# Kernel tuning notes

Hardware: AMD Instinct MI355X
Metric: run time of the kernel (lower is better)

The kernel has to match this reference:

```python
import jax, jax.numpy as jnp
import numpy as np

N, K, D = 65536, 1024, 512


def setup_inputs() -> dict:
    key = jax.random.key(0)
    k1, k2, k3 = jax.random.split(key, 3)
    x = jax.random.normal(k1, (N, D), dtype=jnp.float32)
    y = jax.random.randint(k2, (N,), 0, K)  # true/assigned cluster labels
    centers = jax.random.normal(k3, (K, D), dtype=jnp.float32)  # nn.Parameter
    return {"x": x, "y": y, "centers": centers}


def reference(x, y, centers):
    # caldis: squared euclidean distance from every point to every center.
    # original expand+sub+square+sum without materializing [N, K, D]).
    x2 = jnp.sum(x * x, axis=1, keepdims=True)          # [N, 1]
    c2 = jnp.sum(centers * centers, axis=1)              # [K]
    distance = x2 - 2.0 * (x @ centers.T) + c2           # [N, K]

    # predict: torch.sort(distance)[1][:, 0] == index of the smallest distance
    ynew = jnp.argmin(distance, axis=1)                  # [N]

    # calwei + calloss: one-hot(y) * distance summed == gather distance[i, y[i]]
    loss = jnp.sum(jnp.take_along_axis(distance, y[:, None], axis=1))

    return loss, ynew
```

## Files before the change

### kernel.cpp

```cpp
#include <hip/hip_runtime.h>

#define NPTS 65536
#define KC   1024
#define DD   512

using bf16x8 = __attribute__((ext_vector_type(8))) __bf16;
using f32x4  = __attribute__((ext_vector_type(4))) float;

__device__ __forceinline__ void gld_lds16(const void* g, void* lds_base) {
  __builtin_amdgcn_global_load_lds(
      (const __attribute__((address_space(1))) unsigned int*)(uintptr_t)g,
      (__attribute__((address_space(3))) unsigned int*)(unsigned int)(uintptr_t)lds_base,
      16, 0, 0);
}

__device__ __forceinline__ uint2 pack4(const float4& v) {
  uint2 r;
  r.x = (__float_as_uint(v.x) >> 16) | (__float_as_uint(v.y) & 0xffff0000u);
  r.y = (__float_as_uint(v.z) >> 16) | (__float_as_uint(v.w) & 0xffff0000u);
  return r;
}


__global__ __launch_bounds__(256) void convert_x_loss(
    const float* __restrict__ x, const int* __restrict__ y,
    const float* __restrict__ centers, uint4* __restrict__ xb,
    float* __restrict__ partial) {
  const int w = threadIdx.x >> 6, l = threadIdx.x & 63;
  const int base = blockIdx.x * 64 + w * 16;
  const float4* xf4 = (const float4*)x;
  const float4* cf4 = (const float4*)centers;
  float s = 0.f;
  for (int p = 0; p < 16; p++) {
    const int row = base + p;
    float4 a = xf4[row * 128 + 2 * l];
    float4 b = xf4[row * 128 + 2 * l + 1];
    uint2 pa = pack4(a), pb = pack4(b);
    xb[row * 64 + l] = make_uint4(pa.x, pa.y, pb.x, pb.y);
    const int yr = y[row];
    float4 ca = cf4[yr * 128 + 2 * l];
    float4 cb = cf4[yr * 128 + 2 * l + 1];
    float d0 = a.x - ca.x, d1 = a.y - ca.y, d2 = a.z - ca.z, d3 = a.w - ca.w;
    float d4 = b.x - cb.x, d5 = b.y - cb.y, d6 = b.z - cb.z, d7 = b.w - cb.w;
    s += d0 * d0 + d1 * d1 + d2 * d2 + d3 * d3;
    s += d4 * d4 + d5 * d5 + d6 * d6 + d7 * d7;
  }
#pragma unroll
  for (int off = 32; off; off >>= 1) s += __shfl_down(s, off, 64);
  __shared__ float ps[4];
  if (l == 0) ps[w] = s;
  __syncthreads();
  if (threadIdx.x == 0) partial[blockIdx.x] = ps[0] + ps[1] + ps[2] + ps[3];
}

__global__ __launch_bounds__(256) void convert_c(
    const float* __restrict__ centers, uint4* __restrict__ cb,
    float* __restrict__ c2) {
  const int row = (blockIdx.x * 256 + threadIdx.x) >> 6;
  const int l = threadIdx.x & 63;
  const float4* cf4 = (const float4*)centers;
  float4 a = cf4[row * 128 + 2 * l];
  float4 b = cf4[row * 128 + 2 * l + 1];
  uint2 pa = pack4(a), pb = pack4(b);
  cb[row * 64 + l] = make_uint4(pa.x, pa.y, pb.x, pb.y);
  float s = a.x * a.x + a.y * a.y + a.z * a.z + a.w * a.w +
            b.x * b.x + b.y * b.y + b.z * b.z + b.w * b.w;
#pragma unroll
  for (int off = 32; off; off >>= 1) s += __shfl_down(s, off, 64);
  if (l == 0) c2[row] = s;
}

__global__ __launch_bounds__(256, 2) void gemm_argmin(
    const uint4* __restrict__ xb, const uint4* __restrict__ cb,
    const float* __restrict__ c2, float* __restrict__ ynew_out) {
  __shared__ uint4 As[1024];
  __shared__ uint4 Bs[1024];
  __shared__ float c2s[1024];

  const int t = threadIdx.x;
  const int w = t >> 6, l = t & 63;
  const int wm = w >> 1, wn = w & 1;
  const int q4 = l >> 4, m16 = l & 15;
  const int row0 = blockIdx.x * 128;

#pragma unroll
  for (int i = 0; i < 4; i++) c2s[t + 256 * i] = c2[t + 256 * i];

  const int r_l = l >> 3;
  const int o_l = (l & 7) ^ r_l;
  int aidx[4], bidx[4];
#pragma unroll
  for (int q = 0; q < 4; q++) {
    const int c = w * 4 + q;
    aidx[q] = (row0 + c * 8 + r_l) * 64 + o_l;
    bidx[q] = (c * 8 + r_l) * 64 + o_l;
  }

  const int xr = m16 & 7;

  float best[16];
  int bi_[16];
#pragma unroll
  for (int i = 0; i < 16; i++) { best[i] = 3.4e38f; bi_[i] = 0; }

  for (int n0 = 0; n0 < KC; n0 += 128) {
    f32x4 acc[4][4];
#pragma unroll
    for (int i = 0; i < 4; i++)
#pragma unroll
      for (int j = 0; j < 4; j++) acc[i][j] = (f32x4){0.f, 0.f, 0.f, 0.f};

    const uint4* bbase = cb + n0 * 64;

    for (int ks = 0; ks < 8; ks++) {
      __syncthreads();
#pragma unroll
      for (int q = 0; q < 4; q++) {
        gld_lds16(xb + aidx[q] + ks * 8, &As[(w * 4 + q) * 64]);
        gld_lds16(bbase + bidx[q] + ks * 8, &Bs[(w * 4 + q) * 64]);
      }
      __syncthreads();
#pragma unroll
      for (int kk = 0; kk < 2; kk++) {
        bf16x8 af[4], bf[4];
        const int oct = kk * 4 + q4;
#pragma unroll
        for (int i = 0; i < 4; i++) {
          const int ra = wm * 64 + i * 16 + m16;
          af[i] = *(const bf16x8*)&As[ra * 8 + (oct ^ xr)];
          const int rb = wn * 64 + i * 16 + m16;
          bf[i] = *(const bf16x8*)&Bs[rb * 8 + (oct ^ xr)];
        }
#pragma unroll
        for (int i = 0; i < 4; i++)
#pragma unroll
          for (int j = 0; j < 4; j++)
            acc[i][j] = __builtin_amdgcn_mfma_f32_16x16x32_bf16(af[i], bf[j], acc[i][j], 0, 0, 0);
      }
    }

#pragma unroll
    for (int j = 0; j < 4; j++) {
      const int n = n0 + wn * 64 + j * 16 + m16;
      const float cc = c2s[n];
#pragma unroll
      for (int i = 0; i < 4; i++)
#pragma unroll
        for (int r = 0; r < 4; r++) {
          float v = fmaf(-2.f, acc[i][j][r], cc);
          const int bi = i * 4 + r;
          if (v < best[bi]) { best[bi] = v; bi_[bi] = n; }
        }
    }
  }

#pragma unroll
  for (int bi = 0; bi < 16; bi++) {
    float v = best[bi];
    int idx = bi_[bi];
#pragma unroll
    for (int off = 8; off; off >>= 1) {
      float ov = __shfl_xor(v, off, 64);
      int oi = __shfl_xor(idx, off, 64);
      if (ov < v || (ov == v && oi < idx)) { v = ov; idx = oi; }
    }
    if (m16 == 0) {
      const int m = wm * 64 + (bi >> 2) * 16 + q4 * 4 + (bi & 3);
      ynew_out[row0 + m] = (float)idx;
    }
  }
}

__global__ __launch_bounds__(256) void loss_final(const float* __restrict__ partial,
                                                  float* __restrict__ out) {
  float s = 0.f;
#pragma unroll
  for (int j = 0; j < 4; j++) s += partial[threadIdx.x + 256 * j];
#pragma unroll
  for (int off = 32; off; off >>= 1) s += __shfl_down(s, off, 64);
  __shared__ float ps[4];
  if ((threadIdx.x & 63) == 0) ps[threadIdx.x >> 6] = s;
  __syncthreads();
  if (threadIdx.x == 0) out[0] = ps[0] + ps[1] + ps[2] + ps[3];
}


#define SLOT(row, oct) (16 * (oct) + (((row) & 15) ^ (((oct) & 2) << 1)))

__device__ __forceinline__ void split_pack(const float4& a, const float4& b,
                                           uint4& hi, uint4& lo) {
  float f[8] = {a.x, a.y, a.z, a.w, b.x, b.y, b.z, b.w};
  uint hw[4], lw[4];
#pragma unroll
  for (int i = 0; i < 4; i++) {
    uint e0 = __float_as_uint(f[2 * i]), e1 = __float_as_uint(f[2 * i + 1]);
    hw[i] = (e0 >> 16) | (e1 & 0xffff0000u);
    float l0 = f[2 * i]     - __uint_as_float(e0 & 0xffff0000u);
    float l1 = f[2 * i + 1] - __uint_as_float(e1 & 0xffff0000u);
    lw[i] = (__float_as_uint(l0) >> 16) | (__float_as_uint(l1) & 0xffff0000u);
  }
  hi = make_uint4(hw[0], hw[1], hw[2], hw[3]);
  lo = make_uint4(lw[0], lw[1], lw[2], lw[3]);
}

__global__ __launch_bounds__(256) void c2_kernel(const float* __restrict__ centers,
                                                 float* __restrict__ c2) {
  int wave = (blockIdx.x * 256 + threadIdx.x) >> 6;
  int lane = threadIdx.x & 63;
  const float4* c4 = (const float4*)(centers + (size_t)wave * DD);
  float s = 0.f;
#pragma unroll
  for (int j = 0; j < 2; j++) {
    float4 v = c4[lane + 64 * j];
    s += v.x * v.x + v.y * v.y + v.z * v.z + v.w * v.w;
  }
#pragma unroll
  for (int off = 32; off; off >>= 1) s += __shfl_down(s, off, 64);
  if (lane == 0) c2[wave] = s;
}

__global__ __launch_bounds__(256, 2) void argmin_fb(
    const float* __restrict__ x, const float* __restrict__ centers,
    const float* __restrict__ c2, float* __restrict__ ynew_out) {
  __shared__ uint4 Ah[512], Al[512], Bh[512], Bl[512];
  const int t = threadIdx.x;
  const int w = t >> 6, l = t & 63;
  const int wm = w >> 1, wn = w & 1;
  const size_t row0 = (size_t)blockIdx.x * 128;
  const int srow = t >> 1, h = t & 1;
  const int mt = srow >> 4;
  const int so0 = mt * 64 + SLOT(srow, 2 * h);
  const int so1 = mt * 64 + SLOT(srow, 2 * h + 1);
  const int rs = SLOT(l & 15, l >> 4);
  const float* xp = x + (row0 + srow) * DD + h * 16;
  float best[16];
  int bidx[16];
#pragma unroll
  for (int i = 0; i < 16; i++) { best[i] = 3.4e38f; bidx[i] = 0; }
  for (int n0 = 0; n0 < KC; n0 += 128) {
    const float* bp = centers + (size_t)(n0 + srow) * DD + h * 16;
    f32x4 acc[4][4];
#pragma unroll
    for (int i = 0; i < 4; i++)
#pragma unroll
      for (int j = 0; j < 4; j++) acc[i][j] = (f32x4){0.f, 0.f, 0.f, 0.f};
    float4 ra[4], rb[4];
#pragma unroll
    for (int q = 0; q < 4; q++) {
      ra[q] = *(const float4*)(xp + q * 4);
      rb[q] = *(const float4*)(bp + q * 4);
    }
    for (int ks = 0; ks < 16; ks++) {
      uint4 ah0, al0, ah1, al1, bh0, bl0, bh1, bl1;
      split_pack(ra[0], ra[1], ah0, al0);
      split_pack(ra[2], ra[3], ah1, al1);
      split_pack(rb[0], rb[1], bh0, bl0);
      split_pack(rb[2], rb[3], bh1, bl1);
      __syncthreads();
      Ah[so0] = ah0; Al[so0] = al0;
      Ah[so1] = ah1; Al[so1] = al1;
      Bh[so0] = bh0; Bl[so0] = bl0;
      Bh[so1] = bh1; Bl[so1] = bl1;
      __syncthreads();
      if (ks < 15) {
#pragma unroll
        for (int q = 0; q < 4; q++) {
          ra[q] = *(const float4*)(xp + (ks + 1) * 32 + q * 4);
          rb[q] = *(const float4*)(bp + (ks + 1) * 32 + q * 4);
        }
      }
      bf16x8 afh[4], afl[4], bfh[4], bfl[4];
#pragma unroll
      for (int i = 0; i < 4; i++) {
        afh[i] = *(const bf16x8*)&Ah[(wm * 4 + i) * 64 + rs];
        afl[i] = *(const bf16x8*)&Al[(wm * 4 + i) * 64 + rs];
        bfh[i] = *(const bf16x8*)&Bh[(wn * 4 + i) * 64 + rs];
        bfl[i] = *(const bf16x8*)&Bl[(wn * 4 + i) * 64 + rs];
      }
#pragma unroll
      for (int i = 0; i < 4; i++)
#pragma unroll
        for (int j = 0; j < 4; j++) {
          acc[i][j] = __builtin_amdgcn_mfma_f32_16x16x32_bf16(afh[i], bfh[j], acc[i][j], 0, 0, 0);
          acc[i][j] = __builtin_amdgcn_mfma_f32_16x16x32_bf16(afl[i], bfh[j], acc[i][j], 0, 0, 0);
          acc[i][j] = __builtin_amdgcn_mfma_f32_16x16x32_bf16(afh[i], bfl[j], acc[i][j], 0, 0, 0);
        }
    }
#pragma unroll
    for (int j = 0; j < 4; j++) {
      int n = n0 + wn * 64 + j * 16 + (l & 15);
      float cc = c2[n];
#pragma unroll
      for (int i = 0; i < 4; i++)
#pragma unroll
        for (int r = 0; r < 4; r++) {
          float v = fmaf(-2.f, acc[i][j][r], cc);
          int bi = i * 4 + r;
          if (v < best[bi]) { best[bi] = v; bidx[bi] = n; }
        }
    }
  }
#pragma unroll
  for (int bi = 0; bi < 16; bi++) {
    float v = best[bi];
    int idx = bidx[bi];
#pragma unroll
    for (int off = 8; off; off >>= 1) {
      float ov = __shfl_xor(v, off, 64);
      int oi = __shfl_xor(idx, off, 64);
      if (ov < v || (ov == v && oi < idx)) { v = ov; idx = oi; }
    }
    if ((l & 15) == 0) {
      int m = wm * 64 + (bi >> 2) * 16 + (l >> 4) * 4 + (bi & 3);
      ynew_out[row0 + m] = (float)idx;
    }
  }
}

__global__ __launch_bounds__(256) void loss_partial_fb(
    const float* __restrict__ x, const int* __restrict__ y,
    const float* __restrict__ centers, float* __restrict__ partial) {
  const int w = threadIdx.x >> 6, l = threadIdx.x & 63;
  const int base = blockIdx.x * 64 + w * 16;
  float s = 0.f;
  for (int p = 0; p < 16; p++) {
    int i = base + p;
    const float4* x4 = (const float4*)(x + (size_t)i * DD);
    const float4* c4 = (const float4*)(centers + (size_t)y[i] * DD);
#pragma unroll
    for (int j = 0; j < 2; j++) {
      float4 xv = x4[l + 64 * j], cv = c4[l + 64 * j];
      float dx = xv.x - cv.x, dy = xv.y - cv.y, dz = xv.z - cv.z, dw = xv.w - cv.w;
      s += dx * dx + dy * dy + dz * dz + dw * dw;
    }
  }
#pragma unroll
  for (int off = 32; off; off >>= 1) s += __shfl_down(s, off, 64);
  __shared__ float ps[4];
  if (l == 0) ps[w] = s;
  __syncthreads();
  if (threadIdx.x == 0) partial[blockIdx.x] = ps[0] + ps[1] + ps[2] + ps[3];
}


extern "C" void kernel_launch(void* const* d_in, const int* in_sizes, int n_in,
                              void* d_out, int out_size, void* d_ws, size_t ws_size,
                              hipStream_t stream) {
  const float* x       = (const float*)d_in[0];
  const int*   y       = (const int*)d_in[1];
  const float* centers = (const float*)d_in[2];
  float* out = (float*)d_out;

  const size_t xb_bytes = (size_t)NPTS * DD * 2;
  const size_t cb_bytes = (size_t)KC * DD * 2;
  const size_t need = xb_bytes + cb_bytes + (KC + 1024) * sizeof(float);

  if (ws_size >= need) {
    uint4* xb      = (uint4*)d_ws;
    uint4* cbp     = (uint4*)((char*)d_ws + xb_bytes);
    float* c2      = (float*)((char*)d_ws + xb_bytes + cb_bytes);
    float* partial = c2 + KC;
    convert_c<<<KC / 4, 256, 0, stream>>>(centers, cbp, c2);
    convert_x_loss<<<NPTS / 64, 256, 0, stream>>>(x, y, centers, xb, partial);
    gemm_argmin<<<NPTS / 128, 256, 0, stream>>>(xb, cbp, c2, out + 1);
    loss_final<<<1, 256, 0, stream>>>(partial, out);
  } else {
    float* c2      = (float*)d_ws;
    float* partial = c2 + KC;
    c2_kernel<<<KC / 4, 256, 0, stream>>>(centers, c2);
    argmin_fb<<<NPTS / 128, 256, 0, stream>>>(x, centers, c2, out + 1);
    loss_partial_fb<<<NPTS / 64, 256, 0, stream>>>(x, y, centers, partial);
    loss_final<<<1, 256, 0, stream>>>(partial, out);
  }
}
```

Before: 289.2 us.

## Widen GEMM N-tile to 256 and spread conversion kernel across more blocks

The argmin GEMM now processes 256 centers per outer iteration instead of 128. Each wave computes a 64x128 sub-tile with 32 accumulators, so A fragments are reused across twice as many MFMAs and the A tile is reloaded half as often. The x conversion and loss kernels now give one row per wave instead of 16, launching 16384 blocks for more parallelism, and the partial-sum buffer and final reduction grow to match. The larger accumulator set and doubled B LDS buffer raise register and shared-memory pressure, which may reduce occupancy under the launch bound of 2.

```diff
diff --git a/kernel.cpp b/kernel.cpp
--- a/kernel.cpp
+++ b/kernel.cpp
@@ -27,24 +27,20 @@
     const float* __restrict__ centers, uint4* __restrict__ xb,
     float* __restrict__ partial) {
   const int w = threadIdx.x >> 6, l = threadIdx.x & 63;
-  const int base = blockIdx.x * 64 + w * 16;
-  const float4* xf4 = (const float4*)x;
-  const float4* cf4 = (const float4*)centers;
-  float s = 0.f;
-  for (int p = 0; p < 16; p++) {
-    const int row = base + p;
-    float4 a = xf4[row * 128 + 2 * l];
-    float4 b = xf4[row * 128 + 2 * l + 1];
-    uint2 pa = pack4(a), pb = pack4(b);
-    xb[row * 64 + l] = make_uint4(pa.x, pa.y, pb.x, pb.y);
-    const int yr = y[row];
-    float4 ca = cf4[yr * 128 + 2 * l];
-    float4 cb = cf4[yr * 128 + 2 * l + 1];
-    float d0 = a.x - ca.x, d1 = a.y - ca.y, d2 = a.z - ca.z, d3 = a.w - ca.w;
-    float d4 = b.x - cb.x, d5 = b.y - cb.y, d6 = b.z - cb.z, d7 = b.w - cb.w;
-    s += d0 * d0 + d1 * d1 + d2 * d2 + d3 * d3;
-    s += d4 * d4 + d5 * d5 + d6 * d6 + d7 * d7;
-  }
+  const int row = blockIdx.x * 4 + w;
+  const float4* xr = (const float4*)(x + (size_t)row * DD);
+  float4 a = xr[2 * l];
+  float4 b = xr[2 * l + 1];
+  uint2 pa = pack4(a), pb = pack4(b);
+  xb[row * 64 + l] = make_uint4(pa.x, pa.y, pb.x, pb.y);
+  const int yr = y[row];
+  const float4* cr = (const float4*)(centers + (size_t)yr * DD);
+  float4 ca = cr[2 * l];
+  float4 cb = cr[2 * l + 1];
+  float d0 = a.x - ca.x, d1 = a.y - ca.y, d2 = a.z - ca.z, d3 = a.w - ca.w;
+  float d4 = b.x - cb.x, d5 = b.y - cb.y, d6 = b.z - cb.z, d7 = b.w - cb.w;
+  float s = d0 * d0 + d1 * d1 + d2 * d2 + d3 * d3 +
+            d4 * d4 + d5 * d5 + d6 * d6 + d7 * d7;
 #pragma unroll
   for (int off = 32; off; off >>= 1) s += __shfl_down(s, off, 64);
   __shared__ float ps[4];
@@ -74,7 +70,7 @@
     const uint4* __restrict__ xb, const uint4* __restrict__ cb,
     const float* __restrict__ c2, float* __restrict__ ynew_out) {
   __shared__ uint4 As[1024];
-  __shared__ uint4 Bs[1024];
+  __shared__ uint4 Bs[2048];
   __shared__ float c2s[1024];
 
   const int t = threadIdx.x;
@@ -88,13 +84,14 @@
 
   const int r_l = l >> 3;
   const int o_l = (l & 7) ^ r_l;
-  int aidx[4], bidx[4];
-#pragma unroll
-  for (int q = 0; q < 4; q++) {
-    const int c = w * 4 + q;
-    aidx[q] = (row0 + c * 8 + r_l) * 64 + o_l;
-    bidx[q] = (c * 8 + r_l) * 64 + o_l;
-  }
+  int aidx[4];
+#pragma unroll
+  for (int q = 0; q < 4; q++)
+    aidx[q] = (row0 + (w * 4 + q) * 8 + r_l) * 64 + o_l;
+  int bsrc[8];
+#pragma unroll
+  for (int q = 0; q < 8; q++)
+    bsrc[q] = ((w * 8 + q) * 8 + r_l) * 64 + o_l;
 
   const int xr = m16 & 7;
 
@@ -103,45 +100,47 @@
 #pragma unroll
   for (int i = 0; i < 16; i++) { best[i] = 3.4e38f; bi_[i] = 0; }
 
-  for (int n0 = 0; n0 < KC; n0 += 128) {
-    f32x4 acc[4][4];
+  for (int n0 = 0; n0 < KC; n0 += 256) {
+    f32x4 acc[4][8];
 #pragma unroll
     for (int i = 0; i < 4; i++)
 #pragma unroll
-      for (int j = 0; j < 4; j++) acc[i][j] = (f32x4){0.f, 0.f, 0.f, 0.f};
+      for (int j = 0; j < 8; j++) acc[i][j] = (f32x4){0.f, 0.f, 0.f, 0.f};
 
     const uint4* bbase = cb + n0 * 64;
 
     for (int ks = 0; ks < 8; ks++) {
       __syncthreads();
 #pragma unroll
-      for (int q = 0; q < 4; q++) {
+      for (int q = 0; q < 4; q++)
         gld_lds16(xb + aidx[q] + ks * 8, &As[(w * 4 + q) * 64]);
-        gld_lds16(bbase + bidx[q] + ks * 8, &Bs[(w * 4 + q) * 64]);
-      }
+#pragma unroll
+      for (int q = 0; q < 8; q++)
+        gld_lds16(bbase + bsrc[q] + ks * 8, &Bs[(w * 8 + q) * 64]);
       __syncthreads();
 #pragma unroll
       for (int kk = 0; kk < 2; kk++) {
-        bf16x8 af[4], bf[4];
         const int oct = kk * 4 + q4;
+        bf16x8 af[4];
 #pragma unroll
         for (int i = 0; i < 4; i++) {
           const int ra = wm * 64 + i * 16 + m16;
           af[i] = *(const bf16x8*)&As[ra * 8 + (oct ^ xr)];
-          const int rb = wn * 64 + i * 16 + m16;
-          bf[i] = *(const bf16x8*)&Bs[rb * 8 + (oct ^ xr)];
-        }
-#pragma unroll
-        for (int i = 0; i < 4; i++)
-#pragma unroll
-          for (int j = 0; j < 4; j++)
-            acc[i][j] = __builtin_amdgcn_mfma_f32_16x16x32_bf16(af[i], bf[j], acc[i][j], 0, 0, 0);
+        }
+#pragma unroll
+        for (int j = 0; j < 8; j++) {
+          const int rb = wn * 128 + j * 16 + m16;
+          bf16x8 bf = *(const bf16x8*)&Bs[rb * 8 + (oct ^ xr)];
+#pragma unroll
+          for (int i = 0; i < 4; i++)
+            acc[i][j] = __builtin_amdgcn_mfma_f32_16x16x32_bf16(af[i], bf, acc[i][j], 0, 0, 0);
+        }
       }
     }
 
 #pragma unroll
-    for (int j = 0; j < 4; j++) {
-      const int n = n0 + wn * 64 + j * 16 + m16;
+    for (int j = 0; j < 8; j++) {
+      const int n = n0 + wn * 128 + j * 16 + m16;
       const float cc = c2s[n];
 #pragma unroll
       for (int i = 0; i < 4; i++)
@@ -175,7 +174,7 @@
                                                   float* __restrict__ out) {
   float s = 0.f;
 #pragma unroll
-  for (int j = 0; j < 4; j++) s += partial[threadIdx.x + 256 * j];
+  for (int j = 0; j < 64; j++) s += partial[threadIdx.x + 256 * j];
 #pragma unroll
   for (int off = 32; off; off >>= 1) s += __shfl_down(s, off, 64);
   __shared__ float ps[4];
@@ -321,18 +320,15 @@
     const float* __restrict__ x, const int* __restrict__ y,
     const float* __restrict__ centers, float* __restrict__ partial) {
   const int w = threadIdx.x >> 6, l = threadIdx.x & 63;
-  const int base = blockIdx.x * 64 + w * 16;
+  const int row = blockIdx.x * 4 + w;
+  const float4* x4 = (const float4*)(x + (size_t)row * DD);
+  const float4* c4 = (const float4*)(centers + (size_t)y[row] * DD);
   float s = 0.f;
-  for (int p = 0; p < 16; p++) {
-    int i = base + p;
-    const float4* x4 = (const float4*)(x + (size_t)i * DD);
-    const float4* c4 = (const float4*)(centers + (size_t)y[i] * DD);
-#pragma unroll
-    for (int j = 0; j < 2; j++) {
-      float4 xv = x4[l + 64 * j], cv = c4[l + 64 * j];
-      float dx = xv.x - cv.x, dy = xv.y - cv.y, dz = xv.z - cv.z, dw = xv.w - cv.w;
-      s += dx * dx + dy * dy + dz * dz + dw * dw;
-    }
+#pragma unroll
+  for (int j = 0; j < 2; j++) {
+    float4 xv = x4[2 * l + j], cv = c4[2 * l + j];
+    float dx = xv.x - cv.x, dy = xv.y - cv.y, dz = xv.z - cv.z, dw = xv.w - cv.w;
+    s += dx * dx + dy * dy + dz * dz + dw * dw;
   }
 #pragma unroll
   for (int off = 32; off; off >>= 1) s += __shfl_down(s, off, 64);
@@ -353,7 +349,7 @@
 
   const size_t xb_bytes = (size_t)NPTS * DD * 2;
   const size_t cb_bytes = (size_t)KC * DD * 2;
-  const size_t need = xb_bytes + cb_bytes + (KC + 1024) * sizeof(float);
+  const size_t need = xb_bytes + cb_bytes + (KC + NPTS / 4) * sizeof(float);
 
   if (ws_size >= need) {
     uint4* xb      = (uint4*)d_ws;
@@ -361,7 +357,7 @@
     float* c2      = (float*)((char*)d_ws + xb_bytes + cb_bytes);
     float* partial = c2 + KC;
     convert_c<<<KC / 4, 256, 0, stream>>>(centers, cbp, c2);
-    convert_x_loss<<<NPTS / 64, 256, 0, stream>>>(x, y, centers, xb, partial);
+    convert_x_loss<<<NPTS / 4, 256, 0, stream>>>(x, y, centers, xb, partial);
     gemm_argmin<<<NPTS / 128, 256, 0, stream>>>(xb, cbp, c2, out + 1);
     loss_final<<<1, 256, 0, stream>>>(partial, out);
   } else {
@@ -369,7 +365,7 @@
     float* partial = c2 + KC;
     c2_kernel<<<KC / 4, 256, 0, stream>>>(centers, c2);
     argmin_fb<<<NPTS / 128, 256, 0, stream>>>(x, centers, c2, out + 1);
-    loss_partial_fb<<<NPTS / 64, 256, 0, stream>>>(x, y, centers, partial);
+    loss_partial_fb<<<NPTS / 4, 256, 0, stream>>>(x, y, centers, partial);
     loss_final<<<1, 256, 0, stream>>>(partial, out);
   }
 }
```

Result: faster. 274.0 us (-5.3%).
